# Kernel tuning notes

Hardware: AMD Instinct MI355X
Metric: run time of the kernel (lower is better)

The kernel has to match this reference:

```python
import jax, jax.numpy as jnp
import numpy as np
import math

EPS = 1e-8


def _cdist(x, y):
    # torch.cdist(p=2) with a grad-safe sqrt (0 grad at zero distance)
    d2 = (jnp.sum(x * x, -1)[:, None] + jnp.sum(y * y, -1)[None, :]
          - 2.0 * x @ y.T)
    d2 = jnp.maximum(d2, 0.0)
    pos = d2 > 0
    return jnp.where(pos, jnp.sqrt(jnp.where(pos, d2, 1.0)), 0.0)


def _metric(proj, dim):
    # [B,D,D] rank-1 + identity, symmetrized, Frobenius-normalized
    m = jnp.einsum('bi,bj->bij', proj, proj) / dim
    m = m + jnp.eye(dim, dtype=proj.dtype)[None]
    m = 0.5 * (m + jnp.swapaxes(m, -2, -1))
    fro = jnp.sqrt(jnp.sum(m * m, axis=(-2, -1), keepdims=True))
    return m / (fro + EPS)


def setup_inputs() -> dict:
    key = jax.random.key(0)
    ks = jax.random.split(key, 4)
    B, D = 4096, 128
    return {
        'query_points': jax.random.normal(ks[0], (B, D), jnp.float32),
        'key_points': jax.random.normal(ks[1], (B, D), jnp.float32),
        'Wq': 0.1 * jax.random.normal(ks[2], (D, D), jnp.float32),
        'bq': jnp.zeros((D,), jnp.float32),
        'Wk': 0.1 * jax.random.normal(ks[3], (D, D), jnp.float32),
        'bk': jnp.zeros((D,), jnp.float32),
    }


def reference(query_points, key_points, Wq, bq, Wk, bk):
    D = Wq.shape[0]
    q = query_points @ Wq.T + bq  # [B,D]
    k = key_points @ Wk.T + bk    # [B,D]
    qm = _metric(q, D)            # [B,D,D]
    km = _metric(k, D)
    q_norm = jnp.sqrt(jnp.einsum('bi,bij,bj->b', q, qm, q))
    k_norm = jnp.sqrt(jnp.einsum('bi,bij,bj->b', k, km, k))
    qn = q / (q_norm[:, None] + EPS)
    kn = k / (k_norm[:, None] + EPS)
    dists = _cdist(qn, kn)                       # [B,B]
    sims = 1.0 / (1.0 + dists)
    temperature = math.sqrt(float(D))
    scores = jax.nn.softmax(sims * temperature, axis=-1)
    score_dists = _cdist(scores, scores)
    input_dists = _cdist(query_points, key_points)
    scale = jnp.mean(input_dists) / (jnp.mean(score_dists) + EPS)
    scores = scores * scale
    scores = scores / (jnp.sum(scores, axis=-1, keepdims=True) + EPS)
    return scores
```

## Files before the change

kernel.cpp:

```cpp
#include <hip/hip_runtime.h>
#include <hip/hip_bf16.h>
#include <math.h>

typedef short short8 __attribute__((ext_vector_type(8)));
typedef float floatx4 __attribute__((ext_vector_type(4)));

#define NB 4096
#define DD 128
static constexpr float EPSF = 1e-8f;
static constexpr float TEMP = 11.313708498984760390f;

static __device__ __forceinline__ short f2bf(float f) {
    __hip_bfloat16 h = __float2bfloat16(f);
    union { __hip_bfloat16 h; short s; } u; u.h = h; return u.s;
}
static __device__ __forceinline__ float bf2f(short s) {
    union { __hip_bfloat16 h; short s; } u; u.s = s;
    return __bfloat162float(u.h);
}

static __device__ __forceinline__ short8 load_cvt8(const float* __restrict__ p) {
    float4 a = *(const float4*)p;
    float4 b = *(const float4*)(p + 4);
    short8 o;
    o[0] = f2bf(a.x); o[1] = f2bf(a.y); o[2] = f2bf(a.z); o[3] = f2bf(a.w);
    o[4] = f2bf(b.x); o[5] = f2bf(b.y); o[6] = f2bf(b.z); o[7] = f2bf(b.w);
    return o;
}

static __device__ __forceinline__ int frag_off(int g, int kidx) {
    return ((((g >> 4) * 4 + (kidx >> 5)) * 4 + ((kidx >> 3) & 3)) * 16
            + (g & 15)) * 8 + (kidx & 7);
}

__global__ __launch_bounds__(512) void proj_kernel(
    const float* __restrict__ qp, const float* __restrict__ kp,
    const float* __restrict__ Wq, const float* __restrict__ bq,
    const float* __restrict__ Wk, const float* __restrict__ bk,
    __hip_bfloat16* __restrict__ qn, __hip_bfloat16* __restrict__ kn,
    float* __restrict__ rq, float* __restrict__ rk)
{
    int t = threadIdx.x;
    int b = blockIdx.x;

    int which = b >> 8;
    int row0 = (b & 255) * 16;
    const float* x    = which ? kp : qp;
    const float* W    = which ? Wk : Wq;
    const float* bias = which ? bk : bq;
    short* outv = which ? (short*)kn : (short*)qn;
    float* outr = which ? rk : rq;

    int lane = t & 63, wid = t >> 6;
    int m = lane & 15, quad = lane >> 4;
    int colb = wid * 16;

    floatx4 acc = (floatx4){0.f, 0.f, 0.f, 0.f};

    #pragma unroll
    for (int ks = 0; ks < 4; ++ks) {
        int koff = ks * 32 + quad * 8;
        short8 af  = load_cvt8(x + (row0 + m) * DD + koff);
        short8 bfr = load_cvt8(W + (colb + m) * DD + koff);
        acc = __builtin_amdgcn_mfma_f32_16x16x32_bf16(af, bfr, acc, 0, 0, 0);
    }

    __shared__ float buf[8][16];
    __shared__ float nfb[16];

    float bv = bias[colb + m];

    #pragma unroll
    for (int r = 0; r < 4; ++r) {
        float v = acc[r] + bv;
        acc[r] = v;
        float p = v * v;
        p += __shfl_xor(p, 1); p += __shfl_xor(p, 2);
        p += __shfl_xor(p, 4); p += __shfl_xor(p, 8);
        if (m == 0) buf[wid][quad*4 + r] = p;
    }
    __syncthreads();
    if (t < 16) {
        float s = 0.f;
        #pragma unroll
        for (int w = 0; w < 8; ++w) s += buf[w][t];
        float fro = sqrtf(s*s*(1.0f/16384.0f) + s*(1.0f/64.0f) + 128.0f);
        float qnorm = sqrtf((s*s*(1.0f/128.0f) + s) / (fro + EPSF));
        nfb[t] = 1.0f / (qnorm + EPSF);
    }
    __syncthreads();

    #pragma unroll
    for (int r = 0; r < 4; ++r) {
        int lrow = quad*4 + r;
        int g = row0 + lrow;
        float nf = nfb[lrow];
        float v = acc[r] * nf;
        short sb = f2bf(v);
        outv[frag_off(g, colb + m)] = sb;
        float vf = bf2f(sb);
        float u = vf * vf;
        u += __shfl_xor(u, 1); u += __shfl_xor(u, 2);
        u += __shfl_xor(u, 4); u += __shfl_xor(u, 8);
        if (m == 0) buf[wid][lrow] = u;
    }
    __syncthreads();
    if (t < 16) {
        float s = 0.f;
        #pragma unroll
        for (int w = 0; w < 8; ++w) s += buf[w][t];
        outr[row0 + t] = s;
    }
}

__global__ __launch_bounds__(1024, 4) void score_rows(
    const __hip_bfloat16* __restrict__ qn, const __hip_bfloat16* __restrict__ kn,
    const float* __restrict__ rq, const float* __restrict__ rk,
    float* __restrict__ P)
{
    int lane = threadIdx.x & 63;
    int wid  = threadIdx.x >> 6;
    int m    = lane & 15;
    int quad = lane >> 4;

    int rowblk = blockIdx.x;
    int r0 = rowblk * 16;
    int cs = wid * 256;

    const short* qs  = (const short*)qn;
    const short* kks = (const short*)kn;

    short8 af[4];
    #pragma unroll
    for (int k4 = 0; k4 < 4; ++k4)
        af[k4] = *(const short8*)(qs + ((rowblk*4 + k4)*64 + lane)*8);

    float rqv = rq[r0 + m];

    float rs = 0.f;
    #pragma unroll
    for (int it = 0; it < 4; ++it) {
        #pragma unroll
        for (int ct = 0; ct < 4; ++ct) {
            int colblk = (cs >> 4) + it*4 + ct;
            short8 bfr[4];
            #pragma unroll
            for (int k4 = 0; k4 < 4; ++k4)
                bfr[k4] = *(const short8*)(kks + ((colblk*4 + k4)*64 + lane)*8);
            floatx4 a = (floatx4){0.f, 0.f, 0.f, 0.f};
            #pragma unroll
            for (int k4 = 0; k4 < 4; ++k4)
                a = __builtin_amdgcn_mfma_f32_16x16x32_bf16(bfr[k4], af[k4], a, 0, 0, 0);
            floatx4 rkv = *(const floatx4*)(rk + colblk*16 + quad*4);
            #pragma unroll
            for (int r = 0; r < 4; ++r) {
                float d2 = fmaf(-2.0f, a[r], rqv + rkv[r]);
                float d  = d2 > 0.0f ? __builtin_amdgcn_sqrtf(d2) : 0.0f;
                float e  = __expf(TEMP * __builtin_amdgcn_rcpf(1.0f + d));
                rs += e;
            }
        }
    }

    rs += __shfl_xor(rs, 16);
    rs += __shfl_xor(rs, 32);

    __shared__ float sums[16][16];
    __shared__ float inv[16];
    if (lane < 16) sums[wid][lane] = rs;
    __syncthreads();
    if (threadIdx.x < 16) {
        float s = 0.f;
        #pragma unroll
        for (int w = 0; w < 16; ++w) s += sums[w][threadIdx.x];
        inv[threadIdx.x] = __builtin_amdgcn_rcpf(s + EPSF);
    }
    __syncthreads();

    float invv = inv[m];

    #pragma unroll
    for (int it = 0; it < 4; ++it) {
        #pragma unroll
        for (int ct = 0; ct < 4; ++ct) {
            int colblk = (cs >> 4) + it*4 + ct;
            short8 bfr[4];
            #pragma unroll
            for (int k4 = 0; k4 < 4; ++k4)
                bfr[k4] = *(const short8*)(kks + ((colblk*4 + k4)*64 + lane)*8);
            floatx4 a = (floatx4){0.f, 0.f, 0.f, 0.f};
            #pragma unroll
            for (int k4 = 0; k4 < 4; ++k4)
                a = __builtin_amdgcn_mfma_f32_16x16x32_bf16(bfr[k4], af[k4], a, 0, 0, 0);
            floatx4 rkv = *(const floatx4*)(rk + colblk*16 + quad*4);
            floatx4 o;
            #pragma unroll
            for (int r = 0; r < 4; ++r) {
                float d2 = fmaf(-2.0f, a[r], rqv + rkv[r]);
                float d  = d2 > 0.0f ? __builtin_amdgcn_sqrtf(d2) : 0.0f;
                float e  = __expf(TEMP * __builtin_amdgcn_rcpf(1.0f + d));
                o[r] = e * invv;
            }
            *(floatx4*)(P + (size_t)(r0 + m) * NB
                          + cs + it*64 + ct*16 + quad*4) = o;
        }
    }
}

extern "C" void kernel_launch(void* const* d_in, const int* in_sizes, int n_in,
                              void* d_out, int out_size, void* d_ws, size_t ws_size,
                              hipStream_t stream) {
    const float* qp = (const float*)d_in[0];
    const float* kp = (const float*)d_in[1];
    const float* Wq = (const float*)d_in[2];
    const float* bq = (const float*)d_in[3];
    const float* Wk = (const float*)d_in[4];
    const float* bk = (const float*)d_in[5];
    float* P = (float*)d_out;

    char* ws = (char*)d_ws;
    __hip_bfloat16* qn = (__hip_bfloat16*)ws;
    __hip_bfloat16* kn = (__hip_bfloat16*)(ws + (size_t)NB*DD*2);
    float* rq = (float*)(ws + (size_t)NB*DD*4);
    float* rk = (float*)(ws + (size_t)NB*DD*4 + (size_t)NB*4);

    hipLaunchKernelGGL(proj_kernel, dim3(512), dim3(512), 0, stream,
                       qp, kp, Wq, bq, Wk, bk, qn, kn, rq, rk);
    hipLaunchKernelGGL(score_rows, dim3(256), dim3(1024), 0, stream,
                       qn, kn, rq, rk, P);
}
```

Before: 125.7 us.

## Split score kernel into row-sum and store kernels with column-segment parallelism

Replaces the single fused score kernel (256 blocks of 1024 threads, one row block each) with two kernels that each run 1024 blocks of 512 threads, splitting each 16-row set across four column segments. The first kernel accumulates partial exp row sums into a global buffer with atomics, and the second recomputes the scores and writes normalized output. The aim is to fill more CUs with more, smaller blocks. The cost is an extra memset, an extra kernel launch and a global round trip for the row sums.

```diff
diff --git a/kernel.cpp b/kernel.cpp
--- a/kernel.cpp
+++ b/kernel.cpp
@@ -113,19 +113,23 @@
     }
 }
 
-__global__ __launch_bounds__(1024, 4) void score_rows(
+
+__global__ __launch_bounds__(512, 8) void row_sums(
     const __hip_bfloat16* __restrict__ qn, const __hip_bfloat16* __restrict__ kn,
     const float* __restrict__ rq, const float* __restrict__ rk,
-    float* __restrict__ P)
+    float* __restrict__ rsg)
 {
-    int lane = threadIdx.x & 63;
-    int wid  = threadIdx.x >> 6;
+    int tid  = threadIdx.x;
+    int lane = tid & 63;
+    int wid  = tid >> 6;
     int m    = lane & 15;
     int quad = lane >> 4;
 
-    int rowblk = blockIdx.x;
-    int r0 = rowblk * 16;
-    int cs = wid * 256;
+    int b      = blockIdx.x;
+    int rowset = b >> 2;
+    int colseg = b & 3;
+    int r0 = rowset * 16;
+    int cs = colseg * 1024 + wid * 128;
 
     const short* qs  = (const short*)qn;
     const short* kks = (const short*)kn;
@@ -133,77 +137,95 @@
     short8 af[4];
     #pragma unroll
     for (int k4 = 0; k4 < 4; ++k4)
-        af[k4] = *(const short8*)(qs + ((rowblk*4 + k4)*64 + lane)*8);
+        af[k4] = *(const short8*)(qs + ((rowset*4 + k4)*64 + lane)*8);
 
     float rqv = rq[r0 + m];
 
     float rs = 0.f;
     #pragma unroll
-    for (int it = 0; it < 4; ++it) {
-        #pragma unroll
-        for (int ct = 0; ct < 4; ++ct) {
-            int colblk = (cs >> 4) + it*4 + ct;
-            short8 bfr[4];
-            #pragma unroll
-            for (int k4 = 0; k4 < 4; ++k4)
-                bfr[k4] = *(const short8*)(kks + ((colblk*4 + k4)*64 + lane)*8);
-            floatx4 a = (floatx4){0.f, 0.f, 0.f, 0.f};
-            #pragma unroll
-            for (int k4 = 0; k4 < 4; ++k4)
-                a = __builtin_amdgcn_mfma_f32_16x16x32_bf16(bfr[k4], af[k4], a, 0, 0, 0);
-            floatx4 rkv = *(const floatx4*)(rk + colblk*16 + quad*4);
-            #pragma unroll
-            for (int r = 0; r < 4; ++r) {
-                float d2 = fmaf(-2.0f, a[r], rqv + rkv[r]);
-                float d  = d2 > 0.0f ? __builtin_amdgcn_sqrtf(d2) : 0.0f;
-                float e  = __expf(TEMP * __builtin_amdgcn_rcpf(1.0f + d));
-                rs += e;
-            }
+    for (int t = 0; t < 8; ++t) {
+        int colblk = (cs >> 4) + t;
+        short8 bfr[4];
+        #pragma unroll
+        for (int k4 = 0; k4 < 4; ++k4)
+            bfr[k4] = *(const short8*)(kks + ((colblk*4 + k4)*64 + lane)*8);
+        floatx4 a = (floatx4){0.f, 0.f, 0.f, 0.f};
+        #pragma unroll
+        for (int k4 = 0; k4 < 4; ++k4)
+            a = __builtin_amdgcn_mfma_f32_16x16x32_bf16(bfr[k4], af[k4], a, 0, 0, 0);
+        floatx4 rkv = *(const floatx4*)(rk + colblk*16 + quad*4);
+        #pragma unroll
+        for (int r = 0; r < 4; ++r) {
+            float d2 = fmaf(-2.0f, a[r], rqv + rkv[r]);
+            float d  = d2 > 0.0f ? __builtin_amdgcn_sqrtf(d2) : 0.0f;
+            float e  = __expf(TEMP * __builtin_amdgcn_rcpf(1.0f + d));
+            rs += e;
         }
     }
 
     rs += __shfl_xor(rs, 16);
     rs += __shfl_xor(rs, 32);
 
-    __shared__ float sums[16][16];
-    __shared__ float inv[16];
+    __shared__ float sums[8][16];
     if (lane < 16) sums[wid][lane] = rs;
     __syncthreads();
-    if (threadIdx.x < 16) {
+    if (tid < 16) {
         float s = 0.f;
         #pragma unroll
-        for (int w = 0; w < 16; ++w) s += sums[w][threadIdx.x];
-        inv[threadIdx.x] = __builtin_amdgcn_rcpf(s + EPSF);
-    }
-    __syncthreads();
-
-    float invv = inv[m];
-
-    #pragma unroll
-    for (int it = 0; it < 4; ++it) {
-        #pragma unroll
-        for (int ct = 0; ct < 4; ++ct) {
-            int colblk = (cs >> 4) + it*4 + ct;
-            short8 bfr[4];
-            #pragma unroll
-            for (int k4 = 0; k4 < 4; ++k4)
-                bfr[k4] = *(const short8*)(kks + ((colblk*4 + k4)*64 + lane)*8);
-            floatx4 a = (floatx4){0.f, 0.f, 0.f, 0.f};
-            #pragma unroll
-            for (int k4 = 0; k4 < 4; ++k4)
-                a = __builtin_amdgcn_mfma_f32_16x16x32_bf16(bfr[k4], af[k4], a, 0, 0, 0);
-            floatx4 rkv = *(const floatx4*)(rk + colblk*16 + quad*4);
-            floatx4 o;
-            #pragma unroll
-            for (int r = 0; r < 4; ++r) {
-                float d2 = fmaf(-2.0f, a[r], rqv + rkv[r]);
-                float d  = d2 > 0.0f ? __builtin_amdgcn_sqrtf(d2) : 0.0f;
-                float e  = __expf(TEMP * __builtin_amdgcn_rcpf(1.0f + d));
-                o[r] = e * invv;
-            }
-            *(floatx4*)(P + (size_t)(r0 + m) * NB
-                          + cs + it*64 + ct*16 + quad*4) = o;
+        for (int w = 0; w < 8; ++w) s += sums[w][tid];
+        atomicAdd(&rsg[r0 + tid], s);
+    }
+}
+
+__global__ __launch_bounds__(512, 8) void score_store(
+    const __hip_bfloat16* __restrict__ qn, const __hip_bfloat16* __restrict__ kn,
+    const float* __restrict__ rq, const float* __restrict__ rk,
+    const float* __restrict__ rsg, float* __restrict__ P)
+{
+    int tid  = threadIdx.x;
+    int lane = tid & 63;
+    int wid  = tid >> 6;
+    int m    = lane & 15;
+    int quad = lane >> 4;
+
+    int b      = blockIdx.x;
+    int rowset = b >> 2;
+    int colseg = b & 3;
+    int r0 = rowset * 16;
+    int cs = colseg * 1024 + wid * 128;
+
+    const short* qs  = (const short*)qn;
+    const short* kks = (const short*)kn;
+
+    short8 af[4];
+    #pragma unroll
+    for (int k4 = 0; k4 < 4; ++k4)
+        af[k4] = *(const short8*)(qs + ((rowset*4 + k4)*64 + lane)*8);
+
+    float rqv  = rq[r0 + m];
+    float invv = __builtin_amdgcn_rcpf(rsg[r0 + m] + EPSF);
+
+    #pragma unroll
+    for (int t = 0; t < 8; ++t) {
+        int colblk = (cs >> 4) + t;
+        short8 bfr[4];
+        #pragma unroll
+        for (int k4 = 0; k4 < 4; ++k4)
+            bfr[k4] = *(const short8*)(kks + ((colblk*4 + k4)*64 + lane)*8);
+        floatx4 a = (floatx4){0.f, 0.f, 0.f, 0.f};
+        #pragma unroll
+        for (int k4 = 0; k4 < 4; ++k4)
+            a = __builtin_amdgcn_mfma_f32_16x16x32_bf16(bfr[k4], af[k4], a, 0, 0, 0);
+        floatx4 rkv = *(const floatx4*)(rk + colblk*16 + quad*4);
+        floatx4 o;
+        #pragma unroll
+        for (int r = 0; r < 4; ++r) {
+            float d2 = fmaf(-2.0f, a[r], rqv + rkv[r]);
+            float d  = d2 > 0.0f ? __builtin_amdgcn_sqrtf(d2) : 0.0f;
+            float e  = __expf(TEMP * __builtin_amdgcn_rcpf(1.0f + d));
+            o[r] = e * invv;
         }
+        *(floatx4*)(P + (size_t)(r0 + m) * NB + colblk*16 + quad*4) = o;
     }
 }
 
@@ -221,11 +243,16 @@
     char* ws = (char*)d_ws;
     __hip_bfloat16* qn = (__hip_bfloat16*)ws;
     __hip_bfloat16* kn = (__hip_bfloat16*)(ws + (size_t)NB*DD*2);
-    float* rq = (float*)(ws + (size_t)NB*DD*4);
-    float* rk = (float*)(ws + (size_t)NB*DD*4 + (size_t)NB*4);
+    float* rq  = (float*)(ws + (size_t)NB*DD*4);
+    float* rk  = (float*)(ws + (size_t)NB*DD*4 + (size_t)NB*4);
+    float* rsg = (float*)(ws + (size_t)NB*DD*4 + (size_t)NB*8);
+
+    hipMemsetAsync(rsg, 0, (size_t)NB * sizeof(float), stream);
 
     hipLaunchKernelGGL(proj_kernel, dim3(512), dim3(512), 0, stream,
                        qp, kp, Wq, bq, Wk, bk, qn, kn, rq, rk);
-    hipLaunchKernelGGL(score_rows, dim3(256), dim3(1024), 0, stream,
-                       qn, kn, rq, rk, P);
-}
+    hipLaunchKernelGGL(row_sums, dim3(1024), dim3(512), 0, stream,
+                       qn, kn, rq, rk, rsg);
+    hipLaunchKernelGGL(score_store, dim3(1024), dim3(512), 0, stream,
+                       qn, kn, rq, rk, rsg, P);
+}
```

After: 166.4 us. 1.32x slower.
